# Kernel optimization log

Hardware: AMD Instinct MI355X
Metric: run time of the kernel (lower is better)

The kernel has to match this reference:

```python
import jax, jax.numpy as jnp
import numpy as np

N, D, E = 16384, 1024, 65536
HID, H1, NCLS = 512, 8, 2


def _glorot(key, shape):
    fan = shape[0] + shape[-1]
    return jax.random.normal(key, shape, jnp.float32) * np.sqrt(2.0 / fan)


def setup_inputs() -> dict:
    key = jax.random.key(0)
    ks = jax.random.split(key, 12)
    return {
        "x": jax.random.normal(ks[0], (N, D), jnp.float32),
        "edge_index": jax.random.randint(ks[1], (2, E), 0, N, dtype=jnp.int32),
        # layer 1: GATConv((-1,-1), 512, heads=8, concat=True)
        "W1_src": _glorot(ks[2], (D, H1 * HID)),
        "W1_dst": _glorot(ks[3], (D, H1 * HID)),
        "att1_src": _glorot(ks[4], (H1, HID)),
        "att1_dst": _glorot(ks[5], (H1, HID)),
        "b1": jnp.zeros((H1 * HID,), jnp.float32),
        # layer 2: GATConv((-1,-1), 2, heads=1, concat=False)
        "W2_src": _glorot(ks[6], (H1 * HID, NCLS)),
        "W2_dst": _glorot(ks[7], (H1 * HID, NCLS)),
        "att2_src": _glorot(ks[8], (1, NCLS)),
        "att2_dst": _glorot(ks[9], (1, NCLS)),
        "b2": jnp.zeros((NCLS,), jnp.float32),
    }


def gat_layer(x, src, dst, Ws, Wd, a_s, a_d, b, heads, ch, concat):
    n = x.shape[0]
    hs = (x @ Ws).reshape(n, heads, ch)  # source-transformed feats [N,H,C]
    hd = (x @ Wd).reshape(n, heads, ch)  # dest-transformed feats  [N,H,C]
    al_s = jnp.einsum("nhc,hc->nh", hs, a_s)  # [N,H]
    al_d = jnp.einsum("nhc,hc->nh", hd, a_d)
    logits = jax.nn.leaky_relu(al_s[src] + al_d[dst], 0.2)  # [E,H]
    # segment softmax over incoming edges of each destination node
    m = jax.ops.segment_max(logits, dst, num_segments=n)
    m = jnp.where(jnp.isfinite(m), m, 0.0)
    e = jnp.exp(logits - m[dst])
    denom = jax.ops.segment_sum(e, dst, num_segments=n)
    alpha = e / (denom[dst] + 1e-16)  # [E,H]
    msg = hs[src] * alpha[:, :, None]  # [E,H,C]
    out = jax.ops.segment_sum(msg, dst, num_segments=n)  # [N,H,C]
    out = out.reshape(n, heads * ch) if concat else out.mean(axis=1)
    return out + b


def reference(x, edge_index, W1_src, W1_dst, att1_src, att1_dst, b1,
              W2_src, W2_dst, att2_src, att2_dst, b2):
    n = x.shape[0]
    # PyG GATConv adds self-loops by default
    loops = jnp.arange(n, dtype=edge_index.dtype)
    src = jnp.concatenate([edge_index[0], loops])
    dst = jnp.concatenate([edge_index[1], loops])
    h = gat_layer(x, src, dst, W1_src, W1_dst, att1_src, att1_dst, b1,
                  H1, HID, concat=True)  # [N, 4096]
    out = gat_layer(h, src, dst, W2_src, W2_dst, att2_src, att2_dst, b2,
                    1, NCLS, concat=False)  # [N, 2]
    return out
```

## Files before the change

### kernel.cpp

```cpp
#include <hip/hip_runtime.h>
#include <cstdint>
#include <cstddef>

#define DEV __device__ __forceinline__

typedef __attribute__((ext_vector_type(8))) short bf16x8;
typedef __attribute__((ext_vector_type(4))) float f32x4;

constexpr int N_  = 16384;
constexpr int D_  = 1024;
constexpr int E_  = 65536;
constexpr int ET_ = E_ + N_;
constexpr int H_  = 8;
constexpr int C_  = 512;
constexpr int F_  = 4096;
constexpr int ZS_ = 48;
constexpr int KSPLIT = 2;

DEV unsigned short f2bf(float f){
  unsigned u = __float_as_uint(f);
  unsigned r = u + 0x7FFFu + ((u >> 16) & 1u);
  return (unsigned short)(r >> 16);
}
DEV float lrelu(float x){ return x >= 0.f ? x : 0.2f * x; }
DEV float waveSum(float v){
  #pragma unroll
  for (int o = 32; o > 0; o >>= 1) v += __shfl_xor(v, o);
  return v;
}
DEV int eSRC(const int* ei, int e){ return e < E_ ? ei[e]      : e - E_; }
DEV int eDST(const int* ei, int e){ return e < E_ ? ei[E_ + e] : e - E_; }

__global__ void init_all(uint4* __restrict__ zr, int n16,
                         const float* __restrict__ W2d, const float* __restrict__ a2d,
                         float* __restrict__ wd2){
  int i = blockIdx.x * blockDim.x + threadIdx.x;
  if (i < n16){ uint4 z = {0u,0u,0u,0u}; zr[i] = z; }
  if (i < F_) wd2[i] = W2d[i * 2] * a2d[0] + W2d[i * 2 + 1] * a2d[1];
}

__global__ __launch_bounds__(256) void build_Vcb(
    const float* __restrict__ W1s, const float* __restrict__ W1d,
    const float* __restrict__ a1s, const float* __restrict__ a1d,
    const float* __restrict__ W2s, const float* __restrict__ wd2,
    const float* __restrict__ b1,
    unsigned short* __restrict__ Vb, float* __restrict__ cb){
  int t = threadIdx.x;
  if (blockIdx.x == D_ * H_ / 4){
    __shared__ float red[3][4];
    int w = t >> 6, lane = t & 63;
    float p0 = 0.f, p1 = 0.f, pd = 0.f;
    for (int k = t; k < F_; k += 256){
      float b = b1[k];
      p0 += b * W2s[k * 2]; p1 += b * W2s[k * 2 + 1]; pd += b * wd2[k];
    }
    p0 = waveSum(p0); p1 = waveSum(p1); pd = waveSum(pd);
    if (lane == 0){ red[0][w] = p0; red[1][w] = p1; red[2][w] = pd; }
    __syncthreads();
    if (t == 0){
      cb[0] = red[0][0] + red[0][1] + red[0][2] + red[0][3];
      cb[1] = red[1][0] + red[1][1] + red[1][2] + red[1][3];
      cb[2] = red[2][0] + red[2][1] + red[2][2] + red[2][3];
    }
    return;
  }
  int id = blockIdx.x * 4 + (t >> 6);
  int lane = t & 63;
  int d = id >> 3, h = id & 7;
  float sa = 0.f, sb = 0.f, s0 = 0.f, s1 = 0.f, sd = 0.f;
  #pragma unroll
  for (int i = 0; i < C_ / 64; i++){
    int c = i * 64 + lane;
    int gc = h * C_ + c;
    float ws  = W1s[(size_t)d * F_ + gc];
    float wdv = W1d[(size_t)d * F_ + gc];
    sa += ws * a1s[gc]; sb += wdv * a1d[gc];
    float2 w2 = *reinterpret_cast<const float2*>(W2s + (size_t)gc * 2);
    s0 += ws * w2.x; s1 += ws * w2.y; sd += ws * wd2[gc];
  }
  sa = waveSum(sa); sb = waveSum(sb);
  s0 = waveSum(s0); s1 = waveSum(s1); sd = waveSum(sd);
  if (lane == 0){
    int kc = d >> 5, ks = (d >> 3) & 3, ii = d & 7;
    auto put = [&](int jj, float v){
      int tt = jj >> 4, j = jj & 15;
      Vb[((size_t)(tt * 32 + kc) * 64 + ks * 16 + j) * 8 + ii] = f2bf(v);
    };
    put(h, sa); put(8 + h, sb); put(16 + h, s0); put(24 + h, s1); put(32 + h, sd);
  }
}

__global__ __launch_bounds__(64) void node_mfma(const float* __restrict__ X,
                                                const unsigned short* __restrict__ Vb,
                                                float* __restrict__ Z){
  int lane = threadIdx.x;
  int n0 = blockIdx.x * 16;
  int kh = blockIdx.y;
  int row = lane & 15, ks = lane >> 4;
  f32x4 ac0 = {0.f,0.f,0.f,0.f}, ac1 = ac0, ac2 = ac0;
  const float* xp = X + (size_t)(n0 + row) * D_ + ks * 8;
  constexpr int KC = 32 / KSPLIT;
  #pragma unroll 2
  for (int kk = 0; kk < KC; kk++){
    int kc = kh * KC + kk;
    float4 xa = *reinterpret_cast<const float4*>(xp + kc * 32);
    float4 xb = *reinterpret_cast<const float4*>(xp + kc * 32 + 4);
    bf16x8 a;
    a[0] = (short)f2bf(xa.x); a[1] = (short)f2bf(xa.y);
    a[2] = (short)f2bf(xa.z); a[3] = (short)f2bf(xa.w);
    a[4] = (short)f2bf(xb.x); a[5] = (short)f2bf(xb.y);
    a[6] = (short)f2bf(xb.z); a[7] = (short)f2bf(xb.w);
    bf16x8 b0 = *reinterpret_cast<const bf16x8*>(&Vb[((size_t)( 0 + kc) * 64 + lane) * 8]);
    bf16x8 b1 = *reinterpret_cast<const bf16x8*>(&Vb[((size_t)(32 + kc) * 64 + lane) * 8]);
    bf16x8 b2 = *reinterpret_cast<const bf16x8*>(&Vb[((size_t)(64 + kc) * 64 + lane) * 8]);
    ac0 = __builtin_amdgcn_mfma_f32_16x16x32_bf16(a, b0, ac0, 0, 0, 0);
    ac1 = __builtin_amdgcn_mfma_f32_16x16x32_bf16(a, b1, ac1, 0, 0, 0);
    ac2 = __builtin_amdgcn_mfma_f32_16x16x32_bf16(a, b2, ac2, 0, 0, 0);
  }
  #pragma unroll
  for (int r = 0; r < 4; r++){
    int n = n0 + ks * 4 + r;
    atomicAdd(&Z[(size_t)n * ZS_ +  0 + row], ac0[r]);
    atomicAdd(&Z[(size_t)n * ZS_ + 16 + row], ac1[r]);
    atomicAdd(&Z[(size_t)n * ZS_ + 32 + row], ac2[r]);
  }
}

__global__ void edge_exp1(const int* __restrict__ ei, const float* __restrict__ Z,
                          float* __restrict__ expv, float* __restrict__ den1){
  int t = blockIdx.x * blockDim.x + threadIdx.x;
  if (t >= ET_ * H_) return;
  int e = t >> 3, h = t & 7;
  int s = eSRC(ei, e), d = eDST(ei, e);
  float lg = lrelu(Z[(size_t)s * ZS_ + h] + Z[(size_t)d * ZS_ + 8 + h]);
  float ev = expf(lg);
  expv[e * 8 + h] = ev;
  atomicAdd(&den1[d * 8 + h], ev);
}

__global__ void agg_z(const int* __restrict__ ei, const float* __restrict__ Z,
                      const float* __restrict__ expv, const float* __restrict__ den1,
                      float* __restrict__ s0a, float* __restrict__ s1a,
                      float* __restrict__ sda){
  int e = blockIdx.x * blockDim.x + threadIdx.x;
  if (e >= ET_) return;
  int s = eSRC(ei, e), d = eDST(ei, e);
  float4 ev0 = *reinterpret_cast<const float4*>(expv + e * 8);
  float4 ev1 = *reinterpret_cast<const float4*>(expv + e * 8 + 4);
  float4 dn0 = *reinterpret_cast<const float4*>(den1 + d * 8);
  float4 dn1 = *reinterpret_cast<const float4*>(den1 + d * 8 + 4);
  float al[8];
  al[0] = ev0.x / (dn0.x + 1e-16f); al[1] = ev0.y / (dn0.y + 1e-16f);
  al[2] = ev0.z / (dn0.z + 1e-16f); al[3] = ev0.w / (dn0.w + 1e-16f);
  al[4] = ev1.x / (dn1.x + 1e-16f); al[5] = ev1.y / (dn1.y + 1e-16f);
  al[6] = ev1.z / (dn1.z + 1e-16f); al[7] = ev1.w / (dn1.w + 1e-16f);
  const float* zp = Z + (size_t)s * ZS_;
  float4 z0a = *reinterpret_cast<const float4*>(zp + 16);
  float4 z0b = *reinterpret_cast<const float4*>(zp + 20);
  float4 z1a = *reinterpret_cast<const float4*>(zp + 24);
  float4 z1b = *reinterpret_cast<const float4*>(zp + 28);
  float4 zda = *reinterpret_cast<const float4*>(zp + 32);
  float4 zdb = *reinterpret_cast<const float4*>(zp + 36);
  float p0 = al[0]*z0a.x + al[1]*z0a.y + al[2]*z0a.z + al[3]*z0a.w
           + al[4]*z0b.x + al[5]*z0b.y + al[6]*z0b.z + al[7]*z0b.w;
  float p1 = al[0]*z1a.x + al[1]*z1a.y + al[2]*z1a.z + al[3]*z1a.w
           + al[4]*z1b.x + al[5]*z1b.y + al[6]*z1b.z + al[7]*z1b.w;
  float pd = al[0]*zda.x + al[1]*zda.y + al[2]*zda.z + al[3]*zda.w
           + al[4]*zdb.x + al[5]*zdb.y + al[6]*zdb.z + al[7]*zdb.w;
  atomicAdd(&s0a[d], p0);
  atomicAdd(&s1a[d], p1);
  atomicAdd(&sda[d], pd);
}

__global__ void edge_exp2(const int* __restrict__ ei, const float* __restrict__ s0a,
                          const float* __restrict__ s1a, const float* __restrict__ sda,
                          const float* __restrict__ cb, const float* __restrict__ a2s,
                          const float* __restrict__ b2,
                          float* __restrict__ expv2, float* __restrict__ den2,
                          float* __restrict__ out){
  int e = blockIdx.x * blockDim.x + threadIdx.x;
  if (e >= ET_) return;
  int s = eSRC(ei, e), d = eDST(ei, e);
  float als = (s0a[s] + cb[0]) * a2s[0] + (s1a[s] + cb[1]) * a2s[1];
  float ald = sda[d] + cb[2];
  float ev = expf(lrelu(als + ald));
  expv2[e] = ev;
  atomicAdd(&den2[d], ev);
  if (e < N_){ out[2 * e] = b2[0]; out[2 * e + 1] = b2[1]; }
}

__global__ void aggregate2(const int* __restrict__ ei, const float* __restrict__ expv2,
                           const float* __restrict__ den2, const float* __restrict__ s0a,
                           const float* __restrict__ s1a, const float* __restrict__ cb,
                           float* __restrict__ out){
  int e = blockIdx.x * blockDim.x + threadIdx.x;
  if (e >= ET_) return;
  int s = eSRC(ei, e), d = eDST(ei, e);
  float a = expv2[e] / (den2[d] + 1e-16f);
  atomicAdd(&out[2 * d],     a * (s0a[s] + cb[0]));
  atomicAdd(&out[2 * d + 1], a * (s1a[s] + cb[1]));
}

extern "C" void kernel_launch(void* const* d_in, const int* in_sizes, int n_in,
                              void* d_out, int out_size, void* d_ws, size_t ws_size,
                              hipStream_t stream){
  const float* x   = (const float*)d_in[0];
  const int*   ei  = (const int*)  d_in[1];
  const float* W1s = (const float*)d_in[2];
  const float* W1d = (const float*)d_in[3];
  const float* a1s = (const float*)d_in[4];
  const float* a1d = (const float*)d_in[5];
  const float* b1  = (const float*)d_in[6];
  const float* W2s = (const float*)d_in[7];
  const float* W2d = (const float*)d_in[8];
  const float* a2s = (const float*)d_in[9];
  const float* a2d = (const float*)d_in[10];
  const float* b2  = (const float*)d_in[11];
  float* out = (float*)d_out;

  char* p = (char*)d_ws;
  auto alloc = [&](size_t bytes) -> void* {
    void* r = (void*)p;
    p += (bytes + 255) & ~(size_t)255;
    return r;
  };
  unsigned short* Vb = (unsigned short*)alloc((size_t)3 * 32 * 64 * 8 * 2);
  float* Z     = (float*)alloc((size_t)N_ * ZS_ * 4);
  float* den1  = (float*)alloc((size_t)N_ * H_ * 4);
  float* den2  = (float*)alloc((size_t)N_ * 4);
  float* s0a   = (float*)alloc((size_t)N_ * 4);
  float* s1a   = (float*)alloc((size_t)N_ * 4);
  float* sda   = (float*)alloc((size_t)N_ * 4);
  float* wd2   = (float*)alloc((size_t)F_ * 4);
  float* cb    = (float*)alloc(256);
  float* expv1 = (float*)alloc((size_t)ET_ * H_ * 4);
  float* expv2 = (float*)alloc((size_t)ET_ * 4);

  size_t zrBytes = (size_t)((char*)wd2 - (char*)Vb);
  int n16 = (int)(zrBytes / 16);
  int g1 = (int)((((n16 > F_) ? n16 : F_) + 255) / 256);

  init_all<<<dim3(g1), dim3(256), 0, stream>>>((uint4*)Vb, n16, W2d, a2d, wd2);
  build_Vcb<<<dim3(D_ * H_ / 4 + 1), dim3(256), 0, stream>>>(W1s, W1d, a1s, a1d,
                                                             W2s, wd2, b1, Vb, cb);
  node_mfma<<<dim3(N_ / 16, KSPLIT), dim3(64), 0, stream>>>(x, Vb, Z);
  edge_exp1<<<dim3(ET_ * H_ / 256), dim3(256), 0, stream>>>(ei, Z, expv1, den1);
  agg_z<<<dim3(ET_ / 256), dim3(256), 0, stream>>>(ei, Z, expv1, den1, s0a, s1a, sda);
  edge_exp2<<<dim3(ET_ / 256), dim3(256), 0, stream>>>(ei, s0a, s1a, sda, cb, a2s, b2,
                                                       expv2, den2, out);
  aggregate2<<<dim3(ET_ / 256), dim3(256), 0, stream>>>(ei, expv2, den2, s0a, s1a, cb, out);
}
```

Measured before the change: 74.77 us.

## Fuse init into prep kernel, widen node_mfma blocks, vectorize edge_exp1 per edge

Merges the zero-init and weight-folding kernels into one prep launch that computes W2d·a2d inline instead of staging it through a wd2 buffer. The buffers are reordered so that one contiguous region (Z through sda) can be zeroed, and Vb now sits after that region instead of being cleared. node_mfma now runs four waves per 256-thread block, covering two node groups and both K halves, instead of 64-thread blocks on a 2D grid. edge_exp1 now uses one thread per edge with float4 loads and stores across all 8 heads, replacing one thread per edge-head pair. The aim is to cut launch count and per-thread overhead. The cost is that the zeroing size depends on the hand-set constant NZB matching the buffer layout.

```diff
diff --git a/kernel.cpp b/kernel.cpp
--- a/kernel.cpp
+++ b/kernel.cpp
@@ -16,6 +16,8 @@
 constexpr int F_  = 4096;
 constexpr int ZS_ = 48;
 constexpr int KSPLIT = 2;
+constexpr int NVB = 2048;
+constexpr int NZB = 960;
 
 DEV unsigned short f2bf(float f){
   unsigned u = __float_as_uint(f);
@@ -31,28 +33,53 @@
 DEV int eSRC(const int* ei, int e){ return e < E_ ? ei[e]      : e - E_; }
 DEV int eDST(const int* ei, int e){ return e < E_ ? ei[E_ + e] : e - E_; }
 
-__global__ void init_all(uint4* __restrict__ zr, int n16,
-                         const float* __restrict__ W2d, const float* __restrict__ a2d,
-                         float* __restrict__ wd2){
-  int i = blockIdx.x * blockDim.x + threadIdx.x;
-  if (i < n16){ uint4 z = {0u,0u,0u,0u}; zr[i] = z; }
-  if (i < F_) wd2[i] = W2d[i * 2] * a2d[0] + W2d[i * 2 + 1] * a2d[1];
-}
-
-__global__ __launch_bounds__(256) void build_Vcb(
+__global__ __launch_bounds__(256) void prep(
     const float* __restrict__ W1s, const float* __restrict__ W1d,
     const float* __restrict__ a1s, const float* __restrict__ a1d,
-    const float* __restrict__ W2s, const float* __restrict__ wd2,
-    const float* __restrict__ b1,
-    unsigned short* __restrict__ Vb, float* __restrict__ cb){
+    const float* __restrict__ W2s, const float* __restrict__ W2d,
+    const float* __restrict__ a2d, const float* __restrict__ b1,
+    unsigned short* __restrict__ Vb, float* __restrict__ cb,
+    uint4* __restrict__ zr){
   int t = threadIdx.x;
-  if (blockIdx.x == D_ * H_ / 4){
+  int bx = blockIdx.x;
+  if (bx < NVB){
+    int id = bx * 4 + (t >> 6);
+    int lane = t & 63;
+    int d = id >> 3, h = id & 7;
+    float a2d0 = a2d[0], a2d1 = a2d[1];
+    float sa = 0.f, sb = 0.f, s0 = 0.f, s1 = 0.f, sd = 0.f;
+    #pragma unroll
+    for (int i = 0; i < C_ / 64; i++){
+      int c = i * 64 + lane;
+      int gc = h * C_ + c;
+      float ws  = W1s[(size_t)d * F_ + gc];
+      float wdv = W1d[(size_t)d * F_ + gc];
+      sa += ws * a1s[gc]; sb += wdv * a1d[gc];
+      float2 w2 = *reinterpret_cast<const float2*>(W2s + (size_t)gc * 2);
+      float2 wx = *reinterpret_cast<const float2*>(W2d + (size_t)gc * 2);
+      s0 += ws * w2.x; s1 += ws * w2.y;
+      sd += ws * (wx.x * a2d0 + wx.y * a2d1);
+    }
+    sa = waveSum(sa); sb = waveSum(sb);
+    s0 = waveSum(s0); s1 = waveSum(s1); sd = waveSum(sd);
+    if (lane == 0){
+      int kc = d >> 5, ks = (d >> 3) & 3, ii = d & 7;
+      auto put = [&](int jj, float v){
+        int tt = jj >> 4, j = jj & 15;
+        Vb[((size_t)(tt * 32 + kc) * 64 + ks * 16 + j) * 8 + ii] = f2bf(v);
+      };
+      put(h, sa); put(8 + h, sb); put(16 + h, s0); put(24 + h, s1); put(32 + h, sd);
+    }
+  } else if (bx == NVB){
     __shared__ float red[3][4];
     int w = t >> 6, lane = t & 63;
+    float a2d0 = a2d[0], a2d1 = a2d[1];
     float p0 = 0.f, p1 = 0.f, pd = 0.f;
     for (int k = t; k < F_; k += 256){
       float b = b1[k];
-      p0 += b * W2s[k * 2]; p1 += b * W2s[k * 2 + 1]; pd += b * wd2[k];
+      float2 w2 = *reinterpret_cast<const float2*>(W2s + (size_t)k * 2);
+      float2 wx = *reinterpret_cast<const float2*>(W2d + (size_t)k * 2);
+      p0 += b * w2.x; p1 += b * w2.y; pd += b * (wx.x * a2d0 + wx.y * a2d1);
     }
     p0 = waveSum(p0); p1 = waveSum(p1); pd = waveSum(pd);
     if (lane == 0){ red[0][w] = p0; red[1][w] = p1; red[2][w] = pd; }
@@ -62,40 +89,21 @@
       cb[1] = red[1][0] + red[1][1] + red[1][2] + red[1][3];
       cb[2] = red[2][0] + red[2][1] + red[2][2] + red[2][3];
     }
-    return;
+  } else {
+    int i = (bx - NVB - 1) * 256 + t;
+    uint4 z = {0u, 0u, 0u, 0u};
+    zr[i] = z;
   }
-  int id = blockIdx.x * 4 + (t >> 6);
-  int lane = t & 63;
-  int d = id >> 3, h = id & 7;
-  float sa = 0.f, sb = 0.f, s0 = 0.f, s1 = 0.f, sd = 0.f;
-  #pragma unroll
-  for (int i = 0; i < C_ / 64; i++){
-    int c = i * 64 + lane;
-    int gc = h * C_ + c;
-    float ws  = W1s[(size_t)d * F_ + gc];
-    float wdv = W1d[(size_t)d * F_ + gc];
-    sa += ws * a1s[gc]; sb += wdv * a1d[gc];
-    float2 w2 = *reinterpret_cast<const float2*>(W2s + (size_t)gc * 2);
-    s0 += ws * w2.x; s1 += ws * w2.y; sd += ws * wd2[gc];
-  }
-  sa = waveSum(sa); sb = waveSum(sb);
-  s0 = waveSum(s0); s1 = waveSum(s1); sd = waveSum(sd);
-  if (lane == 0){
-    int kc = d >> 5, ks = (d >> 3) & 3, ii = d & 7;
-    auto put = [&](int jj, float v){
-      int tt = jj >> 4, j = jj & 15;
-      Vb[((size_t)(tt * 32 + kc) * 64 + ks * 16 + j) * 8 + ii] = f2bf(v);
-    };
-    put(h, sa); put(8 + h, sb); put(16 + h, s0); put(24 + h, s1); put(32 + h, sd);
-  }
-}
-
-__global__ __launch_bounds__(64) void node_mfma(const float* __restrict__ X,
-                                                const unsigned short* __restrict__ Vb,
-                                                float* __restrict__ Z){
-  int lane = threadIdx.x;
-  int n0 = blockIdx.x * 16;
-  int kh = blockIdx.y;
+}
+
+__global__ __launch_bounds__(256) void node_mfma(const float* __restrict__ X,
+                                                 const unsigned short* __restrict__ Vb,
+                                                 float* __restrict__ Z){
+  int t = threadIdx.x;
+  int w = t >> 6, lane = t & 63;
+  int ngrp = blockIdx.x * 2 + (w >> 1);
+  int kh = w & 1;
+  int n0 = ngrp * 16;
   int row = lane & 15, ks = lane >> 4;
   f32x4 ac0 = {0.f,0.f,0.f,0.f}, ac1 = ac0, ac2 = ac0;
   const float* xp = X + (size_t)(n0 + row) * D_ + ks * 8;
@@ -128,14 +136,25 @@
 
 __global__ void edge_exp1(const int* __restrict__ ei, const float* __restrict__ Z,
                           float* __restrict__ expv, float* __restrict__ den1){
-  int t = blockIdx.x * blockDim.x + threadIdx.x;
-  if (t >= ET_ * H_) return;
-  int e = t >> 3, h = t & 7;
-  int s = eSRC(ei, e), d = eDST(ei, e);
-  float lg = lrelu(Z[(size_t)s * ZS_ + h] + Z[(size_t)d * ZS_ + 8 + h]);
-  float ev = expf(lg);
-  expv[e * 8 + h] = ev;
-  atomicAdd(&den1[d * 8 + h], ev);
+  int e = blockIdx.x * blockDim.x + threadIdx.x;
+  if (e >= ET_) return;
+  int s = eSRC(ei, e), d = eDST(ei, e);
+  const float4* zs = reinterpret_cast<const float4*>(Z + (size_t)s * ZS_);
+  const float4* zd = reinterpret_cast<const float4*>(Z + (size_t)d * ZS_ + 8);
+  float4 sa0 = zs[0], sa1 = zs[1];
+  float4 da0 = zd[0], da1 = zd[1];
+  float4 ev0, ev1;
+  ev0.x = expf(lrelu(sa0.x + da0.x)); ev0.y = expf(lrelu(sa0.y + da0.y));
+  ev0.z = expf(lrelu(sa0.z + da0.z)); ev0.w = expf(lrelu(sa0.w + da0.w));
+  ev1.x = expf(lrelu(sa1.x + da1.x)); ev1.y = expf(lrelu(sa1.y + da1.y));
+  ev1.z = expf(lrelu(sa1.z + da1.z)); ev1.w = expf(lrelu(sa1.w + da1.w));
+  float4* ep = reinterpret_cast<float4*>(expv + (size_t)e * 8);
+  ep[0] = ev0; ep[1] = ev1;
+  float* dn = den1 + (size_t)d * 8;
+  atomicAdd(dn + 0, ev0.x); atomicAdd(dn + 1, ev0.y);
+  atomicAdd(dn + 2, ev0.z); atomicAdd(dn + 3, ev0.w);
+  atomicAdd(dn + 4, ev1.x); atomicAdd(dn + 5, ev1.y);
+  atomicAdd(dn + 6, ev1.z); atomicAdd(dn + 7, ev1.w);
 }
 
 __global__ void agg_z(const int* __restrict__ ei, const float* __restrict__ Z,
@@ -145,10 +164,10 @@
   int e = blockIdx.x * blockDim.x + threadIdx.x;
   if (e >= ET_) return;
   int s = eSRC(ei, e), d = eDST(ei, e);
-  float4 ev0 = *reinterpret_cast<const float4*>(expv + e * 8);
-  float4 ev1 = *reinterpret_cast<const float4*>(expv + e * 8 + 4);
-  float4 dn0 = *reinterpret_cast<const float4*>(den1 + d * 8);
-  float4 dn1 = *reinterpret_cast<const float4*>(den1 + d * 8 + 4);
+  float4 ev0 = *reinterpret_cast<const float4*>(expv + (size_t)e * 8);
+  float4 ev1 = *reinterpret_cast<const float4*>(expv + (size_t)e * 8 + 4);
+  float4 dn0 = *reinterpret_cast<const float4*>(den1 + (size_t)d * 8);
+  float4 dn1 = *reinterpret_cast<const float4*>(den1 + (size_t)d * 8 + 4);
   float al[8];
   al[0] = ev0.x / (dn0.x + 1e-16f); al[1] = ev0.y / (dn0.y + 1e-16f);
   al[2] = ev0.z / (dn0.z + 1e-16f); al[3] = ev0.w / (dn0.w + 1e-16f);
@@ -224,27 +243,21 @@
     p += (bytes + 255) & ~(size_t)255;
     return r;
   };
-  unsigned short* Vb = (unsigned short*)alloc((size_t)3 * 32 * 64 * 8 * 2);
   float* Z     = (float*)alloc((size_t)N_ * ZS_ * 4);
   float* den1  = (float*)alloc((size_t)N_ * H_ * 4);
   float* den2  = (float*)alloc((size_t)N_ * 4);
   float* s0a   = (float*)alloc((size_t)N_ * 4);
   float* s1a   = (float*)alloc((size_t)N_ * 4);
   float* sda   = (float*)alloc((size_t)N_ * 4);
-  float* wd2   = (float*)alloc((size_t)F_ * 4);
+  unsigned short* Vb = (unsigned short*)alloc((size_t)3 * 32 * 64 * 8 * 2);
   float* cb    = (float*)alloc(256);
   float* expv1 = (float*)alloc((size_t)ET_ * H_ * 4);
   float* expv2 = (float*)alloc((size_t)ET_ * 4);
 
-  size_t zrBytes = (size_t)((char*)wd2 - (char*)Vb);
-  int n16 = (int)(zrBytes / 16);
-  int g1 = (int)((((n16 > F_) ? n16 : F_) + 255) / 256);
-
-  init_all<<<dim3(g1), dim3(256), 0, stream>>>((uint4*)Vb, n16, W2d, a2d, wd2);
-  build_Vcb<<<dim3(D_ * H_ / 4 + 1), dim3(256), 0, stream>>>(W1s, W1d, a1s, a1d,
-                                                             W2s, wd2, b1, Vb, cb);
-  node_mfma<<<dim3(N_ / 16, KSPLIT), dim3(64), 0, stream>>>(x, Vb, Z);
-  edge_exp1<<<dim3(ET_ * H_ / 256), dim3(256), 0, stream>>>(ei, Z, expv1, den1);
+  prep<<<dim3(NVB + 1 + NZB), dim3(256), 0, stream>>>(W1s, W1d, a1s, a1d, W2s, W2d,
+                                                      a2d, b1, Vb, cb, (uint4*)Z);
+  node_mfma<<<dim3(N_ / 32), dim3(256), 0, stream>>>(x, Vb, Z);
+  edge_exp1<<<dim3((ET_ + 255) / 256), dim3(256), 0, stream>>>(ei, Z, expv1, den1);
   agg_z<<<dim3(ET_ / 256), dim3(256), 0, stream>>>(ei, Z, expv1, den1, s0a, s1a, sda);
   edge_exp2<<<dim3(ET_ / 256), dim3(256), 0, stream>>>(ei, s0a, s1a, sda, cb, a2s, b2,
                                                        expv2, den2, out);
```

Measured after the change: 99.02 us. +32.4%, slower.

## Defer softmax normalization to per-node passes and drop per-edge exp buffers

Applied to the files above, without the earlier changes.

Accumulates unnormalized exp-weighted sums per destination node and head, then divides by the denominator in a per-node pass, for both layers. This removes the stored per-edge exp arrays and the second edge pass that reread them. A node-level kernel packs the layer-2 source and destination inputs into one float4 per node. In exchange, the first edge kernel issues four atomics per (edge, head) instead of one, and extra per-node arrays must be zeroed.

```diff
diff --git a/kernel.cpp b/kernel.cpp
--- a/kernel.cpp
+++ b/kernel.cpp
@@ -126,79 +126,66 @@
   }
 }
 
-__global__ void edge_exp1(const int* __restrict__ ei, const float* __restrict__ Z,
-                          float* __restrict__ expv, float* __restrict__ den1){
+__global__ void edge1(const int* __restrict__ ei, const float* __restrict__ Z,
+                      float* __restrict__ den1, float* __restrict__ a0,
+                      float* __restrict__ a1, float* __restrict__ ad){
   int t = blockIdx.x * blockDim.x + threadIdx.x;
   if (t >= ET_ * H_) return;
   int e = t >> 3, h = t & 7;
   int s = eSRC(ei, e), d = eDST(ei, e);
-  float lg = lrelu(Z[(size_t)s * ZS_ + h] + Z[(size_t)d * ZS_ + 8 + h]);
-  float ev = expf(lg);
-  expv[e * 8 + h] = ev;
-  atomicAdd(&den1[d * 8 + h], ev);
-}
-
-__global__ void agg_z(const int* __restrict__ ei, const float* __restrict__ Z,
-                      const float* __restrict__ expv, const float* __restrict__ den1,
-                      float* __restrict__ s0a, float* __restrict__ s1a,
-                      float* __restrict__ sda){
+  const float* zs = Z + (size_t)s * ZS_;
+  float ev = expf(lrelu(zs[h] + Z[(size_t)d * ZS_ + 8 + h]));
+  int o = d * 8 + h;
+  atomicAdd(&den1[o], ev);
+  atomicAdd(&a0[o], ev * zs[16 + h]);
+  atomicAdd(&a1[o], ev * zs[24 + h]);
+  atomicAdd(&ad[o], ev * zs[32 + h]);
+}
+
+__global__ void node_mid(const float* __restrict__ den1, const float* __restrict__ a0,
+                         const float* __restrict__ a1, const float* __restrict__ ad,
+                         const float* __restrict__ cb, const float* __restrict__ a2s,
+                         float4* __restrict__ Pn){
+  int n = blockIdx.x * blockDim.x + threadIdx.x;
+  if (n >= N_) return;
+  float v0 = 0.f, v1 = 0.f, vd = 0.f;
+  #pragma unroll
+  for (int h = 0; h < 8; h++){
+    float inv = 1.f / (den1[n * 8 + h] + 1e-16f);
+    v0 += a0[n * 8 + h] * inv;
+    v1 += a1[n * 8 + h] * inv;
+    vd += ad[n * 8 + h] * inv;
+  }
+  v0 += cb[0]; v1 += cb[1]; vd += cb[2];
+  float4 r;
+  r.x = v0 * a2s[0] + v1 * a2s[1];
+  r.y = v0; r.z = v1;
+  r.w = vd;
+  Pn[n] = r;
+}
+
+__global__ void edge2(const int* __restrict__ ei, const float4* __restrict__ Pn,
+                      float* __restrict__ den2, float* __restrict__ o0,
+                      float* __restrict__ o1){
   int e = blockIdx.x * blockDim.x + threadIdx.x;
   if (e >= ET_) return;
   int s = eSRC(ei, e), d = eDST(ei, e);
-  float4 ev0 = *reinterpret_cast<const float4*>(expv + e * 8);
-  float4 ev1 = *reinterpret_cast<const float4*>(expv + e * 8 + 4);
-  float4 dn0 = *reinterpret_cast<const float4*>(den1 + d * 8);
-  float4 dn1 = *reinterpret_cast<const float4*>(den1 + d * 8 + 4);
-  float al[8];
-  al[0] = ev0.x / (dn0.x + 1e-16f); al[1] = ev0.y / (dn0.y + 1e-16f);
-  al[2] = ev0.z / (dn0.z + 1e-16f); al[3] = ev0.w / (dn0.w + 1e-16f);
-  al[4] = ev1.x / (dn1.x + 1e-16f); al[5] = ev1.y / (dn1.y + 1e-16f);
-  al[6] = ev1.z / (dn1.z + 1e-16f); al[7] = ev1.w / (dn1.w + 1e-16f);
-  const float* zp = Z + (size_t)s * ZS_;
-  float4 z0a = *reinterpret_cast<const float4*>(zp + 16);
-  float4 z0b = *reinterpret_cast<const float4*>(zp + 20);
-  float4 z1a = *reinterpret_cast<const float4*>(zp + 24);
-  float4 z1b = *reinterpret_cast<const float4*>(zp + 28);
-  float4 zda = *reinterpret_cast<const float4*>(zp + 32);
-  float4 zdb = *reinterpret_cast<const float4*>(zp + 36);
-  float p0 = al[0]*z0a.x + al[1]*z0a.y + al[2]*z0a.z + al[3]*z0a.w
-           + al[4]*z0b.x + al[5]*z0b.y + al[6]*z0b.z + al[7]*z0b.w;
-  float p1 = al[0]*z1a.x + al[1]*z1a.y + al[2]*z1a.z + al[3]*z1a.w
-           + al[4]*z1b.x + al[5]*z1b.y + al[6]*z1b.z + al[7]*z1b.w;
-  float pd = al[0]*zda.x + al[1]*zda.y + al[2]*zda.z + al[3]*zda.w
-           + al[4]*zdb.x + al[5]*zdb.y + al[6]*zdb.z + al[7]*zdb.w;
-  atomicAdd(&s0a[d], p0);
-  atomicAdd(&s1a[d], p1);
-  atomicAdd(&sda[d], pd);
-}
-
-__global__ void edge_exp2(const int* __restrict__ ei, const float* __restrict__ s0a,
-                          const float* __restrict__ s1a, const float* __restrict__ sda,
-                          const float* __restrict__ cb, const float* __restrict__ a2s,
-                          const float* __restrict__ b2,
-                          float* __restrict__ expv2, float* __restrict__ den2,
-                          float* __restrict__ out){
-  int e = blockIdx.x * blockDim.x + threadIdx.x;
-  if (e >= ET_) return;
-  int s = eSRC(ei, e), d = eDST(ei, e);
-  float als = (s0a[s] + cb[0]) * a2s[0] + (s1a[s] + cb[1]) * a2s[1];
-  float ald = sda[d] + cb[2];
-  float ev = expf(lrelu(als + ald));
-  expv2[e] = ev;
+  float4 ps = Pn[s];
+  float ald = Pn[d].w;
+  float ev = expf(lrelu(ps.x + ald));
   atomicAdd(&den2[d], ev);
-  if (e < N_){ out[2 * e] = b2[0]; out[2 * e + 1] = b2[1]; }
-}
-
-__global__ void aggregate2(const int* __restrict__ ei, const float* __restrict__ expv2,
-                           const float* __restrict__ den2, const float* __restrict__ s0a,
-                           const float* __restrict__ s1a, const float* __restrict__ cb,
-                           float* __restrict__ out){
-  int e = blockIdx.x * blockDim.x + threadIdx.x;
-  if (e >= ET_) return;
-  int s = eSRC(ei, e), d = eDST(ei, e);
-  float a = expv2[e] / (den2[d] + 1e-16f);
-  atomicAdd(&out[2 * d],     a * (s0a[s] + cb[0]));
-  atomicAdd(&out[2 * d + 1], a * (s1a[s] + cb[1]));
+  atomicAdd(&o0[d], ev * ps.y);
+  atomicAdd(&o1[d], ev * ps.z);
+}
+
+__global__ void node_out(const float* __restrict__ den2, const float* __restrict__ o0,
+                         const float* __restrict__ o1, const float* __restrict__ b2,
+                         float* __restrict__ out){
+  int n = blockIdx.x * blockDim.x + threadIdx.x;
+  if (n >= N_) return;
+  float inv = 1.f / (den2[n] + 1e-16f);
+  out[2 * n]     = o0[n] * inv + b2[0];
+  out[2 * n + 1] = o1[n] * inv + b2[1];
 }
 
 extern "C" void kernel_launch(void* const* d_in, const int* in_sizes, int n_in,
@@ -224,29 +211,29 @@
     p += (bytes + 255) & ~(size_t)255;
     return r;
   };
-  unsigned short* Vb = (unsigned short*)alloc((size_t)3 * 32 * 64 * 8 * 2);
   float* Z     = (float*)alloc((size_t)N_ * ZS_ * 4);
   float* den1  = (float*)alloc((size_t)N_ * H_ * 4);
+  float* a0    = (float*)alloc((size_t)N_ * H_ * 4);
+  float* a1    = (float*)alloc((size_t)N_ * H_ * 4);
+  float* ad    = (float*)alloc((size_t)N_ * H_ * 4);
   float* den2  = (float*)alloc((size_t)N_ * 4);
-  float* s0a   = (float*)alloc((size_t)N_ * 4);
-  float* s1a   = (float*)alloc((size_t)N_ * 4);
-  float* sda   = (float*)alloc((size_t)N_ * 4);
+  float* o0    = (float*)alloc((size_t)N_ * 4);
+  float* o1    = (float*)alloc((size_t)N_ * 4);
+  unsigned short* Vb = (unsigned short*)alloc((size_t)3 * 32 * 64 * 8 * 2);
   float* wd2   = (float*)alloc((size_t)F_ * 4);
   float* cb    = (float*)alloc(256);
-  float* expv1 = (float*)alloc((size_t)ET_ * H_ * 4);
-  float* expv2 = (float*)alloc((size_t)ET_ * 4);
-
-  size_t zrBytes = (size_t)((char*)wd2 - (char*)Vb);
+  float4* Pn   = (float4*)alloc((size_t)N_ * 16);
+
+  size_t zrBytes = (size_t)((char*)wd2 - (char*)Z);
   int n16 = (int)(zrBytes / 16);
   int g1 = (int)((((n16 > F_) ? n16 : F_) + 255) / 256);
 
-  init_all<<<dim3(g1), dim3(256), 0, stream>>>((uint4*)Vb, n16, W2d, a2d, wd2);
+  init_all<<<dim3(g1), dim3(256), 0, stream>>>((uint4*)Z, n16, W2d, a2d, wd2);
   build_Vcb<<<dim3(D_ * H_ / 4 + 1), dim3(256), 0, stream>>>(W1s, W1d, a1s, a1d,
                                                              W2s, wd2, b1, Vb, cb);
   node_mfma<<<dim3(N_ / 16, KSPLIT), dim3(64), 0, stream>>>(x, Vb, Z);
-  edge_exp1<<<dim3(ET_ * H_ / 256), dim3(256), 0, stream>>>(ei, Z, expv1, den1);
-  agg_z<<<dim3(ET_ / 256), dim3(256), 0, stream>>>(ei, Z, expv1, den1, s0a, s1a, sda);
-  edge_exp2<<<dim3(ET_ / 256), dim3(256), 0, stream>>>(ei, s0a, s1a, sda, cb, a2s, b2,
-                                                       expv2, den2, out);
-  aggregate2<<<dim3(ET_ / 256), dim3(256), 0, stream>>>(ei, expv2, den2, s0a, s1a, cb, out);
-}
+  edge1<<<dim3(ET_ * H_ / 256), dim3(256), 0, stream>>>(ei, Z, den1, a0, a1, ad);
+  node_mid<<<dim3(N_ / 256), dim3(256), 0, stream>>>(den1, a0, a1, ad, cb, a2s, Pn);
+  edge2<<<dim3(ET_ / 256), dim3(256), 0, stream>>>(ei, Pn, den2, o0, o1);
+  node_out<<<dim3(N_ / 256), dim3(256), 0, stream>>>(den2, o0, o1, b2, out);
+}
```

New measurement: 73.89 us. Within noise of the previous version (-1.2%).
